# Performance work log

Measured on AMD Instinct MI355X. Metric: run time of the kernel, lower is better.

Reference implementation:

```python
import jax, jax.numpy as jnp
import numpy as np

N, E, G = 100000, 1600000, 256
D, H, O, DEPTH = 128, 128, 128, 3
BN_EPS = 1e-5
LN_EPS = 1e-5


def setup_inputs() -> dict:
    key = jax.random.key(0)
    ks = jax.random.split(key, 16)
    x = jax.random.normal(ks[0], (N, D), dtype=jnp.float32)
    edge_index = jax.random.randint(ks[1], (2, E), 0, N, dtype=jnp.int64)
    batch = jnp.sort(jax.random.randint(ks[2], (N,), 0, G, dtype=jnp.int64))
    s1 = 1.0 / np.sqrt(D)
    s2 = 1.0 / np.sqrt(H)
    return {
        "x": x,
        "edge_index": edge_index,
        "batch": batch,
        "W1s": jax.random.normal(ks[3], (DEPTH, D, H), dtype=jnp.float32) * s1,
        "b1s": jax.random.normal(ks[4], (DEPTH, H), dtype=jnp.float32) * 0.01,
        "bn_g": jnp.ones((DEPTH, H), dtype=jnp.float32),
        "bn_b": jnp.zeros((DEPTH, H), dtype=jnp.float32),
        "bn_m": jax.random.normal(ks[5], (DEPTH, H), dtype=jnp.float32) * 0.1,
        "bn_v": jax.random.uniform(ks[6], (DEPTH, H), dtype=jnp.float32, minval=0.5, maxval=1.5),
        "W2s": jax.random.normal(ks[7], (DEPTH, H, H), dtype=jnp.float32) * s2,
        "b2s": jax.random.normal(ks[8], (DEPTH, H), dtype=jnp.float32) * 0.01,
        "Wp": jax.random.normal(ks[9], (H, O), dtype=jnp.float32) * s2,
        "bp": jax.random.normal(ks[10], (O,), dtype=jnp.float32) * 0.01,
        "ln_g": jnp.ones((O,), dtype=jnp.float32),
        "ln_b": jnp.zeros((O,), dtype=jnp.float32),
    }


def reference(x, edge_index, batch, W1s, b1s, bn_g, bn_b, bn_m, bn_v, W2s, b2s, Wp, bp, ln_g, ln_b):
    src, dst = edge_index[0], edge_index[1]
    h = x
    for l in range(DEPTH):
        # GIN aggregation (eps=0): (1+eps)*h_i + sum_{j->i} h_j
        agg = jax.ops.segment_sum(h[src], dst, num_segments=N)  # [N, H]
        z = h + agg
        # MLP: Linear -> BatchNorm(eval) -> ReLU -> Linear
        z = z @ W1s[l] + b1s[l]
        z = (z - bn_m[l]) * jax.lax.rsqrt(bn_v[l] + BN_EPS) * bn_g[l] + bn_b[l]
        z = jax.nn.relu(z)
        z = z @ W2s[l] + b2s[l]
        # post-conv ReLU (dropout = identity in eval)
        h = jax.nn.relu(z)
    # global mean pool over graphs
    counts = jax.ops.segment_sum(jnp.ones((N,), h.dtype), batch, num_segments=G)
    hg = jax.ops.segment_sum(h, batch, num_segments=G) / jnp.maximum(counts, 1.0)[:, None]
    # proj: Linear + LayerNorm
    p = hg @ Wp + bp
    mu = jnp.mean(p, axis=-1, keepdims=True)
    var = jnp.var(p, axis=-1, keepdims=True)
    return (p - mu) * jax.lax.rsqrt(var + LN_EPS) * ln_g + ln_b
```

## Files before the change

kernel.cpp:

```cpp
#include <hip/hip_runtime.h>
#include <hip/hip_bf16.h>


#define GDEPTH 3
#define CAP 64

typedef __bf16 bf16x8 __attribute__((ext_vector_type(8)));
typedef float  f32x4  __attribute__((ext_vector_type(4)));
typedef __hip_bfloat16  bf16;
typedef __hip_bfloat162 bf162;

#define CSR_CH 8192
#define NSLICE 8
#define NSLICE_LOG 3

__global__ void k_setup(const float* __restrict__ W1s, const float* __restrict__ W2s,
                        const float* __restrict__ b1s, const float* __restrict__ bng,
                        const float* __restrict__ bnb, const float* __restrict__ bnm,
                        const float* __restrict__ bnv,
                        bf16* __restrict__ Wp1, bf16* __restrict__ Wp2,
                        float* __restrict__ sArr, float* __restrict__ tArr,
                        const float4* __restrict__ x4, bf162* __restrict__ h,
                        const int* __restrict__ batch, int* __restrict__ gp,
                        const int* __restrict__ ei, int* __restrict__ fill,
                        int* __restrict__ col,
                        int N, int E, int G, int BCONV, int BGB) {
    int bid = blockIdx.x;
    int tid = threadIdx.x;
    if (bid < 384) {
        int idx = bid * 256 + tid;
        int l   = idx / 32768;
        int rem = idx - l * 32768;
        int w   = rem >> 14;
        int p   = rem & 16383;
        int j = p & 7, n = (p >> 3) & 127, tq = p >> 10;
        int quad = tq & 3, kk = tq >> 2;
        int k = kk * 32 + quad * 8 + j;
        const float* W = w ? W2s : W1s;
        bf16* Wp = w ? Wp2 : Wp1;
        Wp[l * 16384 + p] = __float2bfloat16(W[l * 16384 + k * 128 + n]);
        if (idx < GDEPTH * 128) {
            int ll = idx >> 7, c = idx & 127;
            float inv = rsqrtf(bnv[ll * 128 + c] + 1e-5f);
            float s = inv * bng[ll * 128 + c];
            sArr[idx] = s;
            tArr[idx] = (b1s[ll * 128 + c] - bnm[ll * 128 + c]) * s + bnb[ll * 128 + c];
        }
        return;
    }
    bid -= 384;
    if (bid < BCONV) {
        int i = bid * 256 + tid;
        int n4 = N * 32;
        if (i < n4) {
            float4 v = x4[i];
            bf162 a, b;
            a.x = __float2bfloat16(v.x); a.y = __float2bfloat16(v.y);
            b.x = __float2bfloat16(v.z); b.y = __float2bfloat16(v.w);
            h[2 * i] = a; h[2 * i + 1] = b;
        }
        return;
    }
    bid -= BCONV;
    if (bid < BGB) {
        int i = bid * 256 + tid;
        if (i < N) {
            int b = batch[i];
            if (i == 0) {
                for (int g = 0; g <= b; ++g) gp[g] = 0;
            } else {
                int pb = batch[i - 1];
                if (pb != b) for (int g = pb + 1; g <= b; ++g) gp[g] = i;
            }
            if (i == N - 1) {
                for (int g = b + 1; g <= G; ++g) gp[g] = N;
            }
        }
        return;
    }
    bid -= BGB;
    {
        int s = bid & (NSLICE - 1);
        int chunk = bid >> NSLICE_LOG;
        int lo = (int)((long long)s * N / NSLICE);
        int hi = (int)((long long)(s + 1) * N / NSLICE);
        int baseq = chunk * (CSR_CH / 4);
        const int4* d4p = (const int4*)(ei + E);
        const int4* s4p = (const int4*)ei;
        #pragma unroll
        for (int i = 0; i < CSR_CH / 1024; ++i) {
            int q = baseq + i * 256 + tid;
            int e0 = q * 4;
            if (e0 + 3 < E) {
                int4 d4 = d4p[q];
                if ((d4.x >= lo && d4.x < hi) || (d4.y >= lo && d4.y < hi) ||
                    (d4.z >= lo && d4.z < hi) || (d4.w >= lo && d4.w < hi)) {
                    int4 s4 = s4p[q];
                    if (d4.x >= lo && d4.x < hi) { int p = atomicAdd(&fill[d4.x], 1); if (p < CAP) col[(size_t)d4.x * CAP + p] = s4.x; }
                    if (d4.y >= lo && d4.y < hi) { int p = atomicAdd(&fill[d4.y], 1); if (p < CAP) col[(size_t)d4.y * CAP + p] = s4.y; }
                    if (d4.z >= lo && d4.z < hi) { int p = atomicAdd(&fill[d4.z], 1); if (p < CAP) col[(size_t)d4.z * CAP + p] = s4.z; }
                    if (d4.w >= lo && d4.w < hi) { int p = atomicAdd(&fill[d4.w], 1); if (p < CAP) col[(size_t)d4.w * CAP + p] = s4.w; }
                }
            } else if (e0 < E) {
                for (int e = e0; e < E; ++e) {
                    int d = ei[E + e];
                    if (d >= lo && d < hi) {
                        int p = atomicAdd(&fill[d], 1);
                        if (p < CAP) col[(size_t)d * CAP + p] = ei[e];
                    }
                }
            }
        }
    }
}

__global__ __launch_bounds__(256) void k_layer(const bf16* __restrict__ h,
                                               const int* __restrict__ deg,
                                               const int* __restrict__ col,
                                               const bf16* __restrict__ Bp1,
                                               const bf16* __restrict__ Bp2,
                                               const float* __restrict__ sv,
                                               const float* __restrict__ tv,
                                               const float* __restrict__ b2,
                                               bf16* __restrict__ Out, int M) {
    __shared__ __align__(16) bf16 As[32 * 136];
    const int tid = threadIdx.x;
    const int m0 = blockIdx.x * 32;
    const int grp = tid >> 4, c = tid & 15;
    const bf16x8* h8 = (const bf16x8*)h;

    #pragma unroll
    for (int it = 0; it < 2; ++it) {
        int row = grp * 2 + it;
        int node = m0 + row;
        float acc[8];
        if (node < M) {
            bf16x8 self = h8[(size_t)node * 16 + c];
            #pragma unroll
            for (int k = 0; k < 8; ++k) acc[k] = (float)self[k];
            int d = deg[node]; if (d > CAP) d = CAP;
            const int* cb = col + (size_t)node * CAP;
            int e = 0;
            for (; e + 3 < d; e += 4) {
                int j0 = cb[e], j1 = cb[e + 1], j2 = cb[e + 2], j3 = cb[e + 3];
                bf16x8 v0 = h8[(size_t)j0 * 16 + c];
                bf16x8 v1 = h8[(size_t)j1 * 16 + c];
                bf16x8 v2 = h8[(size_t)j2 * 16 + c];
                bf16x8 v3 = h8[(size_t)j3 * 16 + c];
                #pragma unroll
                for (int k = 0; k < 8; ++k)
                    acc[k] += ((float)v0[k] + (float)v1[k]) + ((float)v2[k] + (float)v3[k]);
            }
            for (; e < d; ++e) {
                bf16x8 v = h8[(size_t)cb[e] * 16 + c];
                #pragma unroll
                for (int k = 0; k < 8; ++k) acc[k] += (float)v[k];
            }
        } else {
            #pragma unroll
            for (int k = 0; k < 8; ++k) acc[k] = 0.f;
        }
        bf16x8 r;
        #pragma unroll
        for (int k = 0; k < 8; ++k) {
            __hip_bfloat16 t = __float2bfloat16(acc[k]);
            r[k] = *(__bf16*)&t;
        }
        *(bf16x8*)(As + row * 136 + c * 8) = r;
    }
    __syncthreads();

    const int lane = tid & 63;
    const int wid = tid >> 6;
    const int wm = wid & 1, wn = wid >> 1;
    const int l15 = lane & 15, quad = lane >> 4;

    f32x4 acc[4];
    #pragma unroll
    for (int j = 0; j < 4; ++j) acc[j] = (f32x4){0.f, 0.f, 0.f, 0.f};
    #pragma unroll
    for (int kk = 0; kk < 4; ++kk) {
        bf16x8 a, b[4];
        #pragma unroll
        for (int tn = 0; tn < 4; ++tn)
            b[tn] = *(const bf16x8*)(Bp1 + ((kk * 4 + quad) * 128 + wn * 64 + tn * 16 + l15) * 8);
        a = *(const bf16x8*)(As + (wm * 16 + l15) * 136 + kk * 32 + quad * 8);
        #pragma unroll
        for (int tn = 0; tn < 4; ++tn)
            acc[tn] = __builtin_amdgcn_mfma_f32_16x16x32_bf16(a, b[tn], acc[tn], 0, 0, 0);
    }
    __syncthreads();
    #pragma unroll
    for (int tn = 0; tn < 4; ++tn) {
        int gc = wn * 64 + tn * 16 + l15;
        float scale = sv[gc], shift = tv[gc];
        #pragma unroll
        for (int r = 0; r < 4; ++r) {
            float v = fmaxf(acc[tn][r] * scale + shift, 0.f);
            int row = wm * 16 + quad * 4 + r;
            __hip_bfloat16 t = __float2bfloat16(v);
            As[row * 136 + gc] = *(bf16*)&t;
        }
    }
    __syncthreads();
    #pragma unroll
    for (int j = 0; j < 4; ++j) acc[j] = (f32x4){0.f, 0.f, 0.f, 0.f};
    #pragma unroll
    for (int kk = 0; kk < 4; ++kk) {
        bf16x8 a, b[4];
        #pragma unroll
        for (int tn = 0; tn < 4; ++tn)
            b[tn] = *(const bf16x8*)(Bp2 + ((kk * 4 + quad) * 128 + wn * 64 + tn * 16 + l15) * 8);
        a = *(const bf16x8*)(As + (wm * 16 + l15) * 136 + kk * 32 + quad * 8);
        #pragma unroll
        for (int tn = 0; tn < 4; ++tn)
            acc[tn] = __builtin_amdgcn_mfma_f32_16x16x32_bf16(a, b[tn], acc[tn], 0, 0, 0);
    }
    #pragma unroll
    for (int tn = 0; tn < 4; ++tn) {
        int gc = wn * 64 + tn * 16 + l15;
        float shift = b2[gc];
        #pragma unroll
        for (int r = 0; r < 4; ++r) {
            int gr = m0 + wm * 16 + quad * 4 + r;
            if (gr < M) {
                float v = fmaxf(acc[tn][r] + shift, 0.f);
                Out[(size_t)gr * 128 + gc] = __float2bfloat16(v);
            }
        }
    }
}

#define PCH 128
__global__ void k_pool(const bf16* __restrict__ h, const int* __restrict__ batch,
                       float* __restrict__ hga, int N) {
    int base = blockIdx.x * PCH;
    if (base >= N) return;
    int t = threadIdx.x;
    int end = base + PCH; if (end > N) end = N;
    int gcur = batch[base];
    float acc = 0.f;
    for (int i = base; i < end; ++i) {
        int g = batch[i];
        if (g != gcur) {
            atomicAdd(&hga[gcur * 128 + t], acc);
            acc = 0.f; gcur = g;
        }
        acc += __bfloat162float(h[(size_t)i * 128 + t]);
    }
    atomicAdd(&hga[gcur * 128 + t], acc);
}

__global__ void k_proj_ln(const float* __restrict__ hga, const int* __restrict__ gp,
                          const float* __restrict__ Wp,
                          const float* __restrict__ bp, const float* __restrict__ lng,
                          const float* __restrict__ lnb, float* __restrict__ out) {
    __shared__ float row[128];
    __shared__ float red[128];
    int g = blockIdx.x, t = threadIdx.x;
    int cntn = gp[g + 1] - gp[g];
    float inv = 1.0f / (float)(cntn < 1 ? 1 : cntn);
    row[t] = hga[g * 128 + t] * inv;
    __syncthreads();
    float p = bp[t];
    #pragma unroll 8
    for (int k = 0; k < 128; ++k) p += row[k] * Wp[k * 128 + t];
    red[t] = p; __syncthreads();
    for (int o = 64; o > 0; o >>= 1) { if (t < o) red[t] += red[t + o]; __syncthreads(); }
    float mu = red[0] * (1.0f / 128.0f);
    __syncthreads();
    float d = p - mu;
    red[t] = d * d; __syncthreads();
    for (int o = 64; o > 0; o >>= 1) { if (t < o) red[t] += red[t + o]; __syncthreads(); }
    float var = red[0] * (1.0f / 128.0f);
    out[g * 128 + t] = d * rsqrtf(var + 1e-5f) * lng[t] + lnb[t];
}

extern "C" void kernel_launch(void* const* d_in, const int* in_sizes, int n_in,
                              void* d_out, int out_size, void* d_ws, size_t ws_size,
                              hipStream_t stream) {
    const float* x   = (const float*)d_in[0];
    const int*   ei  = (const int*)d_in[1];
    const int*   bat = (const int*)d_in[2];
    const float* W1s = (const float*)d_in[3];
    const float* b1s = (const float*)d_in[4];
    const float* bng = (const float*)d_in[5];
    const float* bnb = (const float*)d_in[6];
    const float* bnm = (const float*)d_in[7];
    const float* bnv = (const float*)d_in[8];
    const float* W2s = (const float*)d_in[9];
    const float* b2s = (const float*)d_in[10];
    const float* Wp  = (const float*)d_in[11];
    const float* bp  = (const float*)d_in[12];
    const float* lng = (const float*)d_in[13];
    const float* lnb = (const float*)d_in[14];
    const int E = in_sizes[1] / 2;
    const int N = in_sizes[2];
    const int G = out_size / 128;

    char* w = (char*)d_ws;
    size_t off = 0;
    auto alloc = [&](size_t b) { char* p = w + off; off += (b + 255) & ~(size_t)255; return p; };
    bf16* buf_a = (bf16*)alloc((size_t)N * 128 * 2);
    bf16* buf_b = (bf16*)alloc((size_t)N * 128 * 2);
    int* col   = (int*)alloc(((size_t)N * CAP + 256) * 4);
    int* fill  = (int*)alloc((size_t)N * 4);
    int* gp    = (int*)alloc(2048);
    bf16* Wp1  = (bf16*)alloc((size_t)GDEPTH * 16384 * 2);
    bf16* Wp2  = (bf16*)alloc((size_t)GDEPTH * 16384 * 2);
    float* sA  = (float*)alloc((size_t)GDEPTH * 128 * 4);
    float* tA  = (float*)alloc((size_t)GDEPTH * 128 * 4);
    float* hga = (float*)alloc((size_t)G * 128 * 4);

    hipMemsetAsync(fill, 0, (size_t)N * 4, stream);
    hipMemsetAsync(hga, 0, (size_t)G * 128 * 4, stream);

    const int BCONV = (N * 32 + 255) / 256;
    const int BGB   = (N + 255) / 256;
    const int BCSR  = ((E + CSR_CH - 1) / CSR_CH) * NSLICE;
    k_setup<<<384 + BCONV + BGB + BCSR, 256, 0, stream>>>(
        W1s, W2s, b1s, bng, bnb, bnm, bnv, Wp1, Wp2, sA, tA,
        (const float4*)x, (bf162*)buf_a, bat, gp, ei, fill, col, N, E, G, BCONV, BGB);

    const bf16* hcur = buf_a;
    bf16* hnext = buf_b;
    for (int l = 0; l < GDEPTH; ++l) {
        k_layer<<<(N + 31) / 32, 256, 0, stream>>>(hcur, fill, col,
                                                   Wp1 + (size_t)l * 16384,
                                                   Wp2 + (size_t)l * 16384,
                                                   sA + l * 128, tA + l * 128,
                                                   b2s + l * 128, hnext, N);
        bf16* tmp = hnext; hnext = (bf16*)hcur; hcur = tmp;
    }
    k_pool<<<(N + PCH - 1) / PCH, 128, 0, stream>>>(hcur, bat, hga, N);
    k_proj_ln<<<G, 128, 0, stream>>>(hga, gp, Wp, bp, lng, lnb, (float*)d_out);
}
```

Baseline: 479.4 us.

## Build CSR with per-slice LDS counters in 64 full-scan blocks

CSR construction now uses 64 blocks, each scanning every edge for its own slice of destination nodes. Per-node fill counters live in shared memory and are written out at the end, replacing global atomics and removing the fill memset. The cost is that each block rereads the whole destination array and only 64 blocks do this work. The shared counter array is sized for the current node count.

```diff
diff --git a/kernel.cpp b/kernel.cpp
--- a/kernel.cpp
+++ b/kernel.cpp
@@ -4,15 +4,12 @@
 
 #define GDEPTH 3
 #define CAP 64
+#define NSCAN 64
 
 typedef __bf16 bf16x8 __attribute__((ext_vector_type(8)));
 typedef float  f32x4  __attribute__((ext_vector_type(4)));
 typedef __hip_bfloat16  bf16;
 typedef __hip_bfloat162 bf162;
-
-#define CSR_CH 8192
-#define NSLICE 8
-#define NSLICE_LOG 3
 
 __global__ void k_setup(const float* __restrict__ W1s, const float* __restrict__ W2s,
                         const float* __restrict__ b1s, const float* __restrict__ bng,
@@ -27,6 +24,43 @@
                         int N, int E, int G, int BCONV, int BGB) {
     int bid = blockIdx.x;
     int tid = threadIdx.x;
+    if (bid < NSCAN) {
+        __shared__ int cnt[1600];
+        int s = bid;
+        int lo = (int)((long long)s * N / NSCAN);
+        int hi = (int)((long long)(s + 1) * N / NSCAN);
+        int sz = hi - lo;
+        for (int i = tid; i < sz; i += 256) cnt[i] = 0;
+        __syncthreads();
+        const int4* d4p = (const int4*)(ei + E);
+        const int4* s4p = (const int4*)ei;
+        int nq = E >> 2;
+        for (int q = tid; q < nq; q += 256) {
+            int4 d4 = d4p[q];
+            unsigned ux = (unsigned)(d4.x - lo), uy = (unsigned)(d4.y - lo);
+            unsigned uz = (unsigned)(d4.z - lo), uw = (unsigned)(d4.w - lo);
+            if (ux < (unsigned)sz || uy < (unsigned)sz ||
+                uz < (unsigned)sz || uw < (unsigned)sz) {
+                int4 s4 = s4p[q];
+                if (ux < (unsigned)sz) { int p = atomicAdd(&cnt[ux], 1); if (p < CAP) col[(size_t)d4.x * CAP + p] = s4.x; }
+                if (uy < (unsigned)sz) { int p = atomicAdd(&cnt[uy], 1); if (p < CAP) col[(size_t)d4.y * CAP + p] = s4.y; }
+                if (uz < (unsigned)sz) { int p = atomicAdd(&cnt[uz], 1); if (p < CAP) col[(size_t)d4.z * CAP + p] = s4.z; }
+                if (uw < (unsigned)sz) { int p = atomicAdd(&cnt[uw], 1); if (p < CAP) col[(size_t)d4.w * CAP + p] = s4.w; }
+            }
+        }
+        for (int e = (nq << 2) + tid; e < E; e += 256) {
+            int d = ei[E + e];
+            unsigned u = (unsigned)(d - lo);
+            if (u < (unsigned)sz) {
+                int p = atomicAdd(&cnt[u], 1);
+                if (p < CAP) col[(size_t)d * CAP + p] = ei[e];
+            }
+        }
+        __syncthreads();
+        for (int i = tid; i < sz; i += 256) fill[lo + i] = cnt[i];
+        return;
+    }
+    bid -= NSCAN;
     if (bid < 384) {
         int idx = bid * 256 + tid;
         int l   = idx / 32768;
@@ -77,40 +111,6 @@
             }
         }
         return;
-    }
-    bid -= BGB;
-    {
-        int s = bid & (NSLICE - 1);
-        int chunk = bid >> NSLICE_LOG;
-        int lo = (int)((long long)s * N / NSLICE);
-        int hi = (int)((long long)(s + 1) * N / NSLICE);
-        int baseq = chunk * (CSR_CH / 4);
-        const int4* d4p = (const int4*)(ei + E);
-        const int4* s4p = (const int4*)ei;
-        #pragma unroll
-        for (int i = 0; i < CSR_CH / 1024; ++i) {
-            int q = baseq + i * 256 + tid;
-            int e0 = q * 4;
-            if (e0 + 3 < E) {
-                int4 d4 = d4p[q];
-                if ((d4.x >= lo && d4.x < hi) || (d4.y >= lo && d4.y < hi) ||
-                    (d4.z >= lo && d4.z < hi) || (d4.w >= lo && d4.w < hi)) {
-                    int4 s4 = s4p[q];
-                    if (d4.x >= lo && d4.x < hi) { int p = atomicAdd(&fill[d4.x], 1); if (p < CAP) col[(size_t)d4.x * CAP + p] = s4.x; }
-                    if (d4.y >= lo && d4.y < hi) { int p = atomicAdd(&fill[d4.y], 1); if (p < CAP) col[(size_t)d4.y * CAP + p] = s4.y; }
-                    if (d4.z >= lo && d4.z < hi) { int p = atomicAdd(&fill[d4.z], 1); if (p < CAP) col[(size_t)d4.z * CAP + p] = s4.z; }
-                    if (d4.w >= lo && d4.w < hi) { int p = atomicAdd(&fill[d4.w], 1); if (p < CAP) col[(size_t)d4.w * CAP + p] = s4.w; }
-                }
-            } else if (e0 < E) {
-                for (int e = e0; e < E; ++e) {
-                    int d = ei[E + e];
-                    if (d >= lo && d < hi) {
-                        int p = atomicAdd(&fill[d], 1);
-                        if (p < CAP) col[(size_t)d * CAP + p] = ei[e];
-                    }
-                }
-            }
-        }
     }
 }
 
@@ -312,13 +312,11 @@
     float* tA  = (float*)alloc((size_t)GDEPTH * 128 * 4);
     float* hga = (float*)alloc((size_t)G * 128 * 4);
 
-    hipMemsetAsync(fill, 0, (size_t)N * 4, stream);
     hipMemsetAsync(hga, 0, (size_t)G * 128 * 4, stream);
 
     const int BCONV = (N * 32 + 255) / 256;
     const int BGB   = (N + 255) / 256;
-    const int BCSR  = ((E + CSR_CH - 1) / CSR_CH) * NSLICE;
-    k_setup<<<384 + BCONV + BGB + BCSR, 256, 0, stream>>>(
+    k_setup<<<NSCAN + 384 + BCONV + BGB, 256, 0, stream>>>(
         W1s, W2s, b1s, bng, bnb, bnm, bnv, Wp1, Wp2, sA, tA,
         (const float4*)x, (bf162*)buf_a, bat, gp, ei, fill, col, N, E, G, BCONV, BGB);
 
```

New measurement: 1.431 ms. +198.4%, slower.
